# Optimization experiments

Measured on AMD Instinct MI355X. Metric: run time of the kernel, lower is better.

## Reference

```python
import jax, jax.numpy as jnp
import numpy as np

N, E, S = 10000, 100000, 10            # nodes, edges, message-passing steps
NODE_F, EDGE_F, L, H, OUT = 30, 4, 128, 128, 3


def _mlp(h, W0, b0, W1, b1, W2, b2):
    # Linear->ReLU, Linear->ReLU, Linear (build_mlp with num_hidden_layers=2)
    h = jax.nn.relu(h @ W0 + b0)
    h = jax.nn.relu(h @ W1 + b1)
    return h @ W2 + b2


def _ln(h, g, b):
    # torch.nn.LayerNorm over last dim, eps=1e-5, biased variance
    m = h.mean(-1, keepdims=True)
    v = h.var(-1, keepdims=True)
    return (h - m) * jax.lax.rsqrt(v + 1e-5) * g + b


def setup_inputs():
    key = jax.random.key(0)
    ks = iter(jax.random.split(key, 64))

    def w(shape, fan):
        return jax.random.normal(next(ks), shape, dtype=jnp.float32) / np.float32(np.sqrt(fan))

    d = {}
    d["x"] = jax.random.normal(next(ks), (N, NODE_F), dtype=jnp.float32)
    d["ea"] = jax.random.normal(next(ks), (E, EDGE_F), dtype=jnp.float32)
    d["ei"] = jax.random.randint(next(ks), (2, E), 0, N)
    # encoder node ('en') / edge ('ee') MLP+LayerNorm params
    for pre, fin in (("en", NODE_F), ("ee", EDGE_F)):
        d[pre + "W0"] = w((fin, H), fin); d[pre + "b0"] = jnp.zeros((H,), jnp.float32)
        d[pre + "W1"] = w((H, H), H);     d[pre + "b1"] = jnp.zeros((H,), jnp.float32)
        d[pre + "W2"] = w((H, L), H);     d[pre + "b2"] = jnp.zeros((L,), jnp.float32)
        d[pre + "g"] = jnp.ones((L,), jnp.float32); d[pre + "bt"] = jnp.zeros((L,), jnp.float32)
    # processor edge ('pe', in=3L) / node ('pn', in=2L) params, stacked over S steps
    for pre, fin in (("pe", 3 * L), ("pn", 2 * L)):
        d[pre + "W0"] = w((S, fin, H), fin); d[pre + "b0"] = jnp.zeros((S, H), jnp.float32)
        d[pre + "W1"] = w((S, H, H), H);     d[pre + "b1"] = jnp.zeros((S, H), jnp.float32)
        d[pre + "W2"] = w((S, H, L), H);     d[pre + "b2"] = jnp.zeros((S, L), jnp.float32)
        d[pre + "g"] = jnp.ones((S, L), jnp.float32); d[pre + "bt"] = jnp.zeros((S, L), jnp.float32)
    # decoder MLP (no LayerNorm)
    d["dW0"] = w((L, H), L); d["db0"] = jnp.zeros((H,), jnp.float32)
    d["dW1"] = w((H, H), H); d["db1"] = jnp.zeros((H,), jnp.float32)
    d["dW2"] = w((H, OUT), H); d["db2"] = jnp.zeros((OUT,), jnp.float32)
    return d


def reference(x, ea, ei,
              enW0, enb0, enW1, enb1, enW2, enb2, eng, enbt,
              eeW0, eeb0, eeW1, eeb1, eeW2, eeb2, eeg, eebt,
              peW0, peb0, peW1, peb1, peW2, peb2, peg, pebt,
              pnW0, pnb0, pnW1, pnb1, pnW2, pnb2, png, pnbt,
              dW0, db0, dW1, db1, dW2, db2):
    src, dst = ei[0], ei[1]
    # encode (GraphIndependent)
    hx = _ln(_mlp(x, enW0, enb0, enW1, enb1, enW2, enb2), eng, enbt)   # [N, L]
    he = _ln(_mlp(ea, eeW0, eeb0, eeW1, eeb1, eeW2, eeb2), eeg, eebt)  # [E, L]

    # process: S InteractionNetwork steps with residuals
    def step(carry, p):
        cx, ce = carry
        (eW0, eb0, eW1, eb1, eW2, eb2, eg, ebt,
         nW0, nb0, nW1, nb1, nW2, nb2, ng, nbt) = p
        edge_in = jnp.concatenate([cx[src], cx[dst], ce], axis=-1)     # [E, 3L]
        ue = _ln(_mlp(edge_in, eW0, eb0, eW1, eb1, eW2, eb2), eg, ebt)  # [E, L]
        agg = jax.ops.segment_sum(ue, dst, num_segments=N)              # [N, L]
        un = _ln(_mlp(jnp.concatenate([cx, agg], axis=-1), nW0, nb0, nW1, nb1, nW2, nb2), ng, nbt)
        return (cx + un, ce + ue), None

    (hx, he), _ = jax.lax.scan(
        step, (hx, he),
        (peW0, peb0, peW1, peb1, peW2, peb2, peg, pebt,
         pnW0, pnb0, pnW1, pnb1, pnW2, pnb2, png, pnbt))

    # decode
    return _mlp(hx, dW0, db0, dW1, db1, dW2, db2)  # [N, OUT]
```

## Files before the change

kernel.cpp:

```cpp
#include <hip/hip_runtime.h>


#define NN 10000
#define NE 100000
#define STEPS 10
#define NODE_F 30
#define EDGE_F 4
#define L 128
#define AP 132
#define BP 36

#define WS_STRIDE 136
#define AB_STRIDE 136

typedef __bf16 bf16x8 __attribute__((ext_vector_type(8)));
typedef float f32x4 __attribute__((ext_vector_type(4)));

__device__ __forceinline__ unsigned short f2bf(float f) {
  __bf16 b = (__bf16)f;
  return __builtin_bit_cast(unsigned short, b);
}
__device__ __forceinline__ float bf2f(unsigned short u) {
  return __builtin_bit_cast(float, (unsigned)u << 16);
}


__device__ __forceinline__ void stage_W(unsigned short* __restrict__ Ws,
                                        const unsigned short* __restrict__ Wt,
                                        int K, int sec, int tid) {
#pragma unroll
  for (int p = 0; p < 8; ++p) {
    int u = tid + p * 256;
    int n = u >> 4, kk = u & 15;
    uint4 v = *(const uint4*)(Wt + (size_t)n * K + sec * 128 + kk * 8);
    *(uint4*)&Ws[n * WS_STRIDE + kk * 8] = v;
  }
}


__device__ __forceinline__ void init_acc(f32x4 acc[2][4], const float* __restrict__ b,
                                         int wcol, int l16) {
#pragma unroll
  for (int j = 0; j < 4; ++j) {
    float bv = b[wcol + j * 16 + l16];
#pragma unroll
    for (int i = 0; i < 2; ++i) acc[i][j] = f32x4{bv, bv, bv, bv};
  }
}

__device__ __forceinline__ void layer_gbf(const unsigned short* __restrict__ ap0,
                                          const unsigned short* __restrict__ ap1,
                                          const unsigned short* __restrict__ Ws,
                                          f32x4 acc[2][4], int wcol, int l4, int l16) {
#pragma unroll
  for (int kk = 0; kk < 4; ++kk) {
    bf16x8 af[2];
    af[0] = *(const bf16x8*)(ap0 + kk * 32 + l4 * 8);
    af[1] = *(const bf16x8*)(ap1 + kk * 32 + l4 * 8);
#pragma unroll
    for (int j = 0; j < 4; ++j) {
      bf16x8 bv = *(const bf16x8*)&Ws[(wcol + j * 16 + l16) * WS_STRIDE + kk * 32 + l4 * 8];
#pragma unroll
      for (int i = 0; i < 2; ++i)
        acc[i][j] = __builtin_amdgcn_mfma_f32_16x16x32_bf16(af[i], bv, acc[i][j], 0, 0, 0);
    }
  }
}

__device__ __forceinline__ void layer_lds(const unsigned short* __restrict__ Ab,
                                          const unsigned short* __restrict__ Ws,
                                          f32x4 acc[2][4], int wrow, int wcol, int l4, int l16) {
#pragma unroll
  for (int kk = 0; kk < 4; ++kk) {
    bf16x8 af[2];
#pragma unroll
    for (int i = 0; i < 2; ++i)
      af[i] = *(const bf16x8*)&Ab[(wrow + i * 16 + l16) * AB_STRIDE + kk * 32 + l4 * 8];
#pragma unroll
    for (int j = 0; j < 4; ++j) {
      bf16x8 bv = *(const bf16x8*)&Ws[(wcol + j * 16 + l16) * WS_STRIDE + kk * 32 + l4 * 8];
#pragma unroll
      for (int i = 0; i < 2; ++i)
        acc[i][j] = __builtin_amdgcn_mfma_f32_16x16x32_bf16(af[i], bv, acc[i][j], 0, 0, 0);
    }
  }
}

__device__ __forceinline__ void relu_to_Ab(unsigned short* __restrict__ Ab, f32x4 acc[2][4],
                                           int wrow, int wcol, int l4, int l16) {
#pragma unroll
  for (int i = 0; i < 2; ++i)
#pragma unroll
    for (int j = 0; j < 4; ++j)
#pragma unroll
      for (int r = 0; r < 4; ++r) {
        int row = wrow + i * 16 + l4 * 4 + r;
        int col = wcol + j * 16 + l16;
        Ab[row * AB_STRIDE + col] = f2bf(fmaxf(acc[i][j][r], 0.f));
      }
}

__device__ __forceinline__ void ln_partials(const f32x4 acc[2][4], float ps[2][4], float ps2[2][4]) {
#pragma unroll
  for (int i = 0; i < 2; ++i)
#pragma unroll
    for (int r = 0; r < 4; ++r) {
      float s = 0.f, s2 = 0.f;
#pragma unroll
      for (int j = 0; j < 4; ++j) { float v = acc[i][j][r]; s += v; s2 += v * v; }
#pragma unroll
      for (int off = 1; off < 16; off <<= 1) {
        s += __shfl_xor(s, off, 64);
        s2 += __shfl_xor(s2, off, 64);
      }
      ps[i][r] = s; ps2[i][r] = s2;
    }
}


__device__ __forceinline__ void init_acc1(f32x4 acc[4], const float bv[4]) {
#pragma unroll
  for (int j = 0; j < 4; ++j) acc[j] = f32x4{bv[j], bv[j], bv[j], bv[j]};
}

__device__ __forceinline__ void layer_gbf1(const unsigned short* __restrict__ ap,
                                           const unsigned short* __restrict__ Ws,
                                           f32x4 acc[4], int wcol, int l4, int l16) {
#pragma unroll
  for (int kk = 0; kk < 4; ++kk) {
    bf16x8 af = *(const bf16x8*)(ap + kk * 32 + l4 * 8);
#pragma unroll
    for (int j = 0; j < 4; ++j) {
      bf16x8 bv = *(const bf16x8*)&Ws[(wcol + j * 16 + l16) * WS_STRIDE + kk * 32 + l4 * 8];
      acc[j] = __builtin_amdgcn_mfma_f32_16x16x32_bf16(af, bv, acc[j], 0, 0, 0);
    }
  }
}

__device__ __forceinline__ void layer_lds1(const unsigned short* __restrict__ Ab,
                                           const unsigned short* __restrict__ Ws,
                                           f32x4 acc[4], int wrow, int wcol, int l4, int l16) {
#pragma unroll
  for (int kk = 0; kk < 4; ++kk) {
    bf16x8 af = *(const bf16x8*)&Ab[(wrow + l16) * AB_STRIDE + kk * 32 + l4 * 8];
#pragma unroll
    for (int j = 0; j < 4; ++j) {
      bf16x8 bv = *(const bf16x8*)&Ws[(wcol + j * 16 + l16) * WS_STRIDE + kk * 32 + l4 * 8];
      acc[j] = __builtin_amdgcn_mfma_f32_16x16x32_bf16(af, bv, acc[j], 0, 0, 0);
    }
  }
}

__device__ __forceinline__ void relu_to_Ab1(unsigned short* __restrict__ Ab, f32x4 acc[4],
                                            int wrow, int wcol, int l4, int l16) {
#pragma unroll
  for (int j = 0; j < 4; ++j)
#pragma unroll
    for (int r = 0; r < 4; ++r) {
      int row = wrow + l4 * 4 + r;
      int col = wcol + j * 16 + l16;
      Ab[row * AB_STRIDE + col] = f2bf(fmaxf(acc[j][r], 0.f));
    }
}

__device__ __forceinline__ void ln_partials1(const f32x4 acc[4], float ps[4], float ps2[4]) {
#pragma unroll
  for (int r = 0; r < 4; ++r) {
    float s = 0.f, s2 = 0.f;
#pragma unroll
    for (int j = 0; j < 4; ++j) { float v = acc[j][r]; s += v; s2 += v * v; }
#pragma unroll
    for (int off = 1; off < 16; off <<= 1) {
      s += __shfl_xor(s, off, 64);
      s2 += __shfl_xor(s2, off, 64);
    }
    ps[r] = s; ps2[r] = s2;
  }
}


__global__ __launch_bounds__(256) void deg_kernel(const int* __restrict__ ei, int* __restrict__ cnt) {
  int e = blockIdx.x * 256 + threadIdx.x;
  if (e < NE) atomicAdd(&cnt[ei[NE + e]], 1);
}

__global__ __launch_bounds__(256) void scan_kernel(const int* __restrict__ cnt,
                                                   int* __restrict__ off, int* __restrict__ cur) {
  __shared__ int sums[256];
  int t = threadIdx.x;
  int base = t * 40;
  int local = 0;
  for (int i = 0; i < 40; ++i) { int n = base + i; if (n < NN) local += cnt[n]; }
  sums[t] = local;
  __syncthreads();
  int val = local;
  for (int d = 1; d < 256; d <<= 1) {
    int add = (t >= d) ? sums[t - d] : 0;
    __syncthreads();
    sums[t] += add;
    __syncthreads();
  }
  int run = sums[t] - val;
  for (int i = 0; i < 40; ++i) {
    int n = base + i;
    if (n < NN) { off[n] = run; cur[n] = run; run += cnt[n]; }
  }
  if (t == 255) off[NN] = sums[255];
}

__global__ __launch_bounds__(256) void scatter_kernel(const int* __restrict__ ei,
                                                      int* __restrict__ cur, int* __restrict__ eid) {
  int e = blockIdx.x * 256 + threadIdx.x;
  if (e < NE) { int p = atomicAdd(&cur[ei[NE + e]], 1); eid[p] = e; }
}


__global__ __launch_bounds__(256) void edge_step_mfma(
    const unsigned short* __restrict__ hx_bf, unsigned short* __restrict__ he_bf,
    unsigned short* __restrict__ ue_bf,
    const int* __restrict__ ei,
    const unsigned short* __restrict__ W0t, const float* __restrict__ b0,
    const unsigned short* __restrict__ W1t, const float* __restrict__ b1,
    const unsigned short* __restrict__ W2t, const float* __restrict__ b2,
    const float* __restrict__ g, const float* __restrict__ bt) {
  __shared__ __align__(16) unsigned short Ws[128 * WS_STRIDE];
  __shared__ __align__(16) unsigned short Ab[64 * AB_STRIDE];
  __shared__ int sidx[64], didx[64];
  int tid = threadIdx.x;
  int w = tid >> 6, lane = tid & 63;
  int l4 = lane >> 4, l16 = lane & 15;
  int wrow = (w >> 1) * 32, wcol = (w & 1) * 64;
  int e0 = blockIdx.x * 64;
  if (tid < 64) {
    int e = min(e0 + tid, NE - 1);
    sidx[tid] = ei[e];
    didx[tid] = ei[NE + e];
  }
  f32x4 acc[2][4];
  init_acc(acc, b0, wcol, l16);
  __syncthreads();
  for (int sec = 0; sec < 3; ++sec) {
    stage_W(Ws, W0t, 384, sec, tid);
    const unsigned short* ap[2];
#pragma unroll
    for (int i = 0; i < 2; ++i) {
      int r = wrow + i * 16 + l16;
      if (sec == 0)      ap[i] = hx_bf + (size_t)sidx[r] * L;
      else if (sec == 1) ap[i] = hx_bf + (size_t)didx[r] * L;
      else               ap[i] = he_bf + (size_t)min(e0 + r, NE - 1) * L;
    }
    __syncthreads();
    layer_gbf(ap[0], ap[1], Ws, acc, wcol, l4, l16);
    __syncthreads();
  }
  relu_to_Ab(Ab, acc, wrow, wcol, l4, l16);
  stage_W(Ws, W1t, 128, 0, tid);
  init_acc(acc, b1, wcol, l16);
  __syncthreads();
  layer_lds(Ab, Ws, acc, wrow, wcol, l4, l16);
  __syncthreads();
  relu_to_Ab(Ab, acc, wrow, wcol, l4, l16);
  stage_W(Ws, W2t, 128, 0, tid);
  init_acc(acc, b2, wcol, l16);
  __syncthreads();
  layer_lds(Ab, Ws, acc, wrow, wcol, l4, l16);
  float ps[2][4], ps2[2][4];
  ln_partials(acc, ps, ps2);
  __syncthreads();
  float* red = (float*)Ab;
  if (l16 == 0) {
#pragma unroll
    for (int i = 0; i < 2; ++i)
#pragma unroll
      for (int r = 0; r < 4; ++r) {
        int row = wrow + i * 16 + l4 * 4 + r;
        red[(w & 1) * 128 + row * 2 + 0] = ps[i][r];
        red[(w & 1) * 128 + row * 2 + 1] = ps2[i][r];
      }
  }
  __syncthreads();
  float gv[4], btv[4];
#pragma unroll
  for (int j = 0; j < 4; ++j) {
    int col = wcol + j * 16 + l16;
    gv[j] = g[col]; btv[j] = bt[col];
  }
#pragma unroll
  for (int i = 0; i < 2; ++i)
#pragma unroll
    for (int r = 0; r < 4; ++r) {
      int row = wrow + i * 16 + l4 * 4 + r;
      float s  = red[row * 2]     + red[128 + row * 2];
      float s2 = red[row * 2 + 1] + red[128 + row * 2 + 1];
      float m = s * (1.f / 128.f);
      float inv = rsqrtf(s2 * (1.f / 128.f) - m * m + 1e-5f);
      int e = e0 + row;
      if (e < NE) {
        size_t hoff = (size_t)e * L;
#pragma unroll
        for (int j = 0; j < 4; ++j) {
          int col = wcol + j * 16 + l16;
          float u = (acc[i][j][r] - m) * inv * gv[j] + btv[j];
          unsigned short old = he_bf[hoff + col];
          he_bf[hoff + col] = f2bf(bf2f(old) + u);
          ue_bf[hoff + col] = f2bf(u);
        }
      }
    }
}


__global__ __launch_bounds__(256) void node_step_mfma(
    float* __restrict__ hx, unsigned short* __restrict__ hx_bf,
    const unsigned short* __restrict__ ue_bf,
    const int* __restrict__ off, const int* __restrict__ eid,
    const unsigned short* __restrict__ W0t, const float* __restrict__ b0,
    const unsigned short* __restrict__ W1t, const float* __restrict__ b1,
    const unsigned short* __restrict__ W2t, const float* __restrict__ b2,
    const float* __restrict__ g, const float* __restrict__ bt) {
  __shared__ __align__(16) unsigned short Ws[128 * WS_STRIDE];
  __shared__ __align__(16) unsigned short Ab[32 * AB_STRIDE];
  __shared__ __align__(16) unsigned short Ag[32 * AB_STRIDE];
  int tid = threadIdx.x;
  int w = tid >> 6, lane = tid & 63;
  int l4 = lane >> 4, l16 = lane & 15;
  int wrow = (w >> 1) * 16, wcol = (w & 1) * 64;
  int n0 = blockIdx.x * 32;
  {
    int r = tid >> 3;
    int cseg = (tid & 7) * 16;
    int n = n0 + r;
    float a[16];
#pragma unroll
    for (int q = 0; q < 16; ++q) a[q] = 0.f;
    if (n < NN) {
      int p0 = off[n], p1 = off[n + 1];
      for (int p = p0; p < p1; ++p) {
        const unsigned short* row = ue_bf + (size_t)eid[p] * L + cseg;
#pragma unroll
        for (int q = 0; q < 2; ++q) {
          uint4 v = *(const uint4*)(row + q * 8);
          a[q * 8 + 0] += __builtin_bit_cast(float, v.x << 16);
          a[q * 8 + 1] += __builtin_bit_cast(float, v.x & 0xffff0000u);
          a[q * 8 + 2] += __builtin_bit_cast(float, v.y << 16);
          a[q * 8 + 3] += __builtin_bit_cast(float, v.y & 0xffff0000u);
          a[q * 8 + 4] += __builtin_bit_cast(float, v.z << 16);
          a[q * 8 + 5] += __builtin_bit_cast(float, v.z & 0xffff0000u);
          a[q * 8 + 6] += __builtin_bit_cast(float, v.w << 16);
          a[q * 8 + 7] += __builtin_bit_cast(float, v.w & 0xffff0000u);
        }
      }
    }
#pragma unroll
    for (int q = 0; q < 8; ++q) {
      unsigned o = (unsigned)f2bf(a[2 * q]) | ((unsigned)f2bf(a[2 * q + 1]) << 16);
      *(unsigned*)&Ag[r * AB_STRIDE + cseg + 2 * q] = o;
    }
  }
  float bv0[4], bv1[4], bv2[4], gv[4], btv[4];
#pragma unroll
  for (int j = 0; j < 4; ++j) {
    int c = wcol + j * 16 + l16;
    bv0[j] = b0[c]; bv1[j] = b1[c]; bv2[j] = b2[c]; gv[j] = g[c]; btv[j] = bt[c];
  }
  stage_W(Ws, W0t, 256, 0, tid);
  f32x4 acc[4];
  init_acc1(acc, bv0);
  __syncthreads();
  {
    const unsigned short* ap = hx_bf + (size_t)min(n0 + wrow + l16, NN - 1) * L;
    layer_gbf1(ap, Ws, acc, wcol, l4, l16);
  }
  __syncthreads();
  stage_W(Ws, W0t, 256, 1, tid);
  __syncthreads();
  layer_lds1(Ag, Ws, acc, wrow, wcol, l4, l16);
  __syncthreads();
  relu_to_Ab1(Ab, acc, wrow, wcol, l4, l16);
  stage_W(Ws, W1t, 128, 0, tid);
  init_acc1(acc, bv1);
  __syncthreads();
  layer_lds1(Ab, Ws, acc, wrow, wcol, l4, l16);
  __syncthreads();
  relu_to_Ab1(Ab, acc, wrow, wcol, l4, l16);
  stage_W(Ws, W2t, 128, 0, tid);
  init_acc1(acc, bv2);
  __syncthreads();
  layer_lds1(Ab, Ws, acc, wrow, wcol, l4, l16);
  float ps[4], ps2[4];
  ln_partials1(acc, ps, ps2);
  __syncthreads();
  float* red = (float*)Ab;
  if (l16 == 0) {
#pragma unroll
    for (int r = 0; r < 4; ++r) {
      int row = wrow + l4 * 4 + r;
      red[(w & 1) * 64 + row * 2 + 0] = ps[r];
      red[(w & 1) * 64 + row * 2 + 1] = ps2[r];
    }
  }
  __syncthreads();
#pragma unroll
  for (int r = 0; r < 4; ++r) {
    int row = wrow + l4 * 4 + r;
    float s  = red[row * 2]     + red[64 + row * 2];
    float s2 = red[row * 2 + 1] + red[64 + row * 2 + 1];
    float m = s * (1.f / 128.f);
    float inv = rsqrtf(s2 * (1.f / 128.f) - m * m + 1e-5f);
    int n = n0 + row;
    if (n < NN) {
#pragma unroll
      for (int j = 0; j < 4; ++j) {
        int col = wcol + j * 16 + l16;
        float un = (acc[j][r] - m) * inv * gv[j] + btv[j];
        float nv = hx[(size_t)n * L + col] + un;
        hx[(size_t)n * L + col] = nv;
        hx_bf[(size_t)n * L + col] = f2bf(nv);
      }
    }
  }
}


__global__ __launch_bounds__(256) void enc_edge_mfma(
    const float* __restrict__ ea,
    const float* __restrict__ W0, const float* __restrict__ b0,
    const unsigned short* __restrict__ W1t, const float* __restrict__ b1,
    const unsigned short* __restrict__ W2t, const float* __restrict__ b2,
    const float* __restrict__ g, const float* __restrict__ bt,
    unsigned short* __restrict__ he_bf) {
  __shared__ __align__(16) unsigned short Ws[128 * WS_STRIDE];
  __shared__ __align__(16) unsigned short Ab[64 * AB_STRIDE];
  int tid = threadIdx.x;
  int w = tid >> 6, lane = tid & 63;
  int l4 = lane >> 4, l16 = lane & 15;
  int wrow = (w >> 1) * 32, wcol = (w & 1) * 64;
  int e0 = blockIdx.x * 64;
  {
    int row = tid >> 2, cbase = (tid & 3) * 32;
    int e = min(e0 + row, NE - 1);
    float4 eav = *(const float4*)&ea[(size_t)e * 4];
#pragma unroll
    for (int c = 0; c < 32; ++c) {
      int col = cbase + c;
      float sum = b0[col] + eav.x * W0[col] + eav.y * W0[128 + col] +
                  eav.z * W0[256 + col] + eav.w * W0[384 + col];
      Ab[row * AB_STRIDE + col] = f2bf(fmaxf(sum, 0.f));
    }
  }
  stage_W(Ws, W1t, 128, 0, tid);
  f32x4 acc[2][4];
  init_acc(acc, b1, wcol, l16);
  __syncthreads();
  layer_lds(Ab, Ws, acc, wrow, wcol, l4, l16);
  __syncthreads();
  relu_to_Ab(Ab, acc, wrow, wcol, l4, l16);
  stage_W(Ws, W2t, 128, 0, tid);
  init_acc(acc, b2, wcol, l16);
  __syncthreads();
  layer_lds(Ab, Ws, acc, wrow, wcol, l4, l16);
  float ps[2][4], ps2[2][4];
  ln_partials(acc, ps, ps2);
  __syncthreads();
  float* red = (float*)Ws;
  if (l16 == 0) {
#pragma unroll
    for (int i = 0; i < 2; ++i)
#pragma unroll
      for (int r = 0; r < 4; ++r) {
        int row = wrow + i * 16 + l4 * 4 + r;
        red[(w & 1) * 128 + row * 2 + 0] = ps[i][r];
        red[(w & 1) * 128 + row * 2 + 1] = ps2[i][r];
      }
  }
  __syncthreads();
  float gv[4], btv[4];
#pragma unroll
  for (int j = 0; j < 4; ++j) {
    int col = wcol + j * 16 + l16;
    gv[j] = g[col]; btv[j] = bt[col];
  }
#pragma unroll
  for (int i = 0; i < 2; ++i)
#pragma unroll
    for (int r = 0; r < 4; ++r) {
      int row = wrow + i * 16 + l4 * 4 + r;
      float s  = red[row * 2]     + red[128 + row * 2];
      float s2 = red[row * 2 + 1] + red[128 + row * 2 + 1];
      float m = s * (1.f / 128.f);
      float inv = rsqrtf(s2 * (1.f / 128.f) - m * m + 1e-5f);
      int e = e0 + row;
      if (e < NE) {
#pragma unroll
        for (int j = 0; j < 4; ++j) {
          int col = wcol + j * 16 + l16;
          he_bf[(size_t)e * L + col] = f2bf((acc[i][j][r] - m) * inv * gv[j] + btv[j]);
        }
      }
    }
}


__global__ __launch_bounds__(256) void wprep_kernel(
    const float* __restrict__ W0, const float* __restrict__ W1, const float* __restrict__ W2,
    unsigned short* __restrict__ out, int K0, int steps) {
  int per_step = 128 * (K0 + 256);
  int idx = blockIdx.x * 256 + threadIdx.x;
  if (idx >= steps * per_step) return;
  int s = idx / per_step, r = idx - s * per_step;
  float v;
  if (r < 128 * K0) {
    int n = r / K0, k = r - n * K0;
    v = W0[(size_t)s * K0 * 128 + (size_t)k * 128 + n];
  } else {
    r -= 128 * K0;
    const float* W = (r < 16384) ? W1 : W2;
    r &= 16383;
    int n = r >> 7, k = r & 127;
    v = W[(size_t)s * 16384 + k * 128 + n];
  }
  out[idx] = f2bf(v);
}

__global__ __launch_bounds__(256) void tprep_kernel(
    const float* __restrict__ W1, const float* __restrict__ W2, unsigned short* __restrict__ out) {
  int idx = blockIdx.x * 256 + threadIdx.x;
  const float* W = (idx < 16384) ? W1 : W2;
  int r = idx & 16383;
  int n = r >> 7, k = r & 127;
  out[idx] = f2bf(W[k * 128 + n]);
}


__device__ __forceinline__ void load_B(float* __restrict__ Bs, const float* __restrict__ W,
                                       int K, int k0, int tid) {
#pragma unroll
  for (int p = 0; p < 16; ++p) {
    int idx = tid + p * 256;
    int kk = idx >> 7;
    int c = idx & 127;
    float v = 0.f;
    if (k0 + kk < K) v = W[(size_t)(k0 + kk) * L + c];
    Bs[c * BP + kk] = v;
  }
}

__device__ __forceinline__ void fma32(const float* __restrict__ As, const float* __restrict__ Bs,
                                      float acc[4][8], int ty, int tx, int koff) {
#pragma unroll
  for (int kk = 0; kk < 32; kk += 4) {
    float4 a[4];
    float4 b[8];
#pragma unroll
    for (int i = 0; i < 4; ++i)
      a[i] = *(const float4*)&As[(ty + 16 * i) * AP + koff + kk];
#pragma unroll
    for (int j = 0; j < 8; ++j)
      b[j] = *(const float4*)&Bs[(tx + 16 * j) * BP + kk];
#pragma unroll
    for (int i = 0; i < 4; ++i)
#pragma unroll
      for (int j = 0; j < 8; ++j) {
        acc[i][j] = fmaf(a[i].x, b[j].x, acc[i][j]);
        acc[i][j] = fmaf(a[i].y, b[j].y, acc[i][j]);
        acc[i][j] = fmaf(a[i].z, b[j].z, acc[i][j]);
        acc[i][j] = fmaf(a[i].w, b[j].w, acc[i][j]);
      }
  }
}

__device__ __forceinline__ void init_bias(float acc[4][8], const float* __restrict__ b, int tx) {
#pragma unroll
  for (int j = 0; j < 8; ++j) {
    float bv = b[tx + 16 * j];
#pragma unroll
    for (int i = 0; i < 4; ++i) acc[i][j] = bv;
  }
}

__device__ __forceinline__ void store_relu(float* __restrict__ As, float acc[4][8], int ty, int tx) {
#pragma unroll
  for (int i = 0; i < 4; ++i)
#pragma unroll
    for (int j = 0; j < 8; ++j)
      As[(ty + 16 * i) * AP + tx + 16 * j] = fmaxf(acc[i][j], 0.f);
}

__device__ __forceinline__ void layer_As(const float* __restrict__ As, float* __restrict__ Bs,
                                         const float* __restrict__ W, const float* __restrict__ bias,
                                         int K, float acc[4][8], int tid, int ty, int tx) {
  init_bias(acc, bias, tx);
  int nc = (K + 31) >> 5;
  for (int bc = 0; bc < nc; ++bc) {
    __syncthreads();
    load_B(Bs, W, K, bc * 32, tid);
    __syncthreads();
    fma32(As, Bs, acc, ty, tx, bc * 32);
  }
}

__device__ __forceinline__ void fillA_gather(float* __restrict__ As, const float* __restrict__ base,
                                             const int* __restrict__ ridx, int tid) {
#pragma unroll
  for (int p = 0; p < 8; ++p) {
    int idx = tid + p * 256;
    int r = idx >> 5;
    int c4 = idx & 31;
    float4 v = *(const float4*)&base[(size_t)ridx[r] * L + c4 * 4];
    *(float4*)&As[r * AP + c4 * 4] = v;
  }
}

__device__ __forceinline__ void lnorm(float acc[4][8], const float* __restrict__ g,
                                      const float* __restrict__ bt, int tx) {
  float gv[8], bv[8];
#pragma unroll
  for (int j = 0; j < 8; ++j) { gv[j] = g[tx + 16 * j]; bv[j] = bt[tx + 16 * j]; }
#pragma unroll
  for (int i = 0; i < 4; ++i) {
    float s = 0.f, s2 = 0.f;
#pragma unroll
    for (int j = 0; j < 8; ++j) { s += acc[i][j]; s2 += acc[i][j] * acc[i][j]; }
#pragma unroll
    for (int off = 1; off < 16; off <<= 1) {
      s  += __shfl_xor(s, off, 64);
      s2 += __shfl_xor(s2, off, 64);
    }
    float m = s * (1.f / 128.f);
    float var = s2 * (1.f / 128.f) - m * m;
    float inv = rsqrtf(var + 1e-5f);
#pragma unroll
    for (int j = 0; j < 8; ++j) acc[i][j] = (acc[i][j] - m) * inv * gv[j] + bv[j];
  }
}

__global__ __launch_bounds__(256) void enc_node_kernel(
    const float* __restrict__ x,
    const float* __restrict__ W0, const float* __restrict__ b0,
    const float* __restrict__ W1, const float* __restrict__ b1,
    const float* __restrict__ W2, const float* __restrict__ b2,
    const float* __restrict__ g, const float* __restrict__ bt,
    float* __restrict__ hx, unsigned short* __restrict__ hx_bf) {
  __shared__ float As[64 * AP];
  __shared__ float Bs[128 * BP];
  int tid = threadIdx.x, ty = tid >> 4, tx = tid & 15;
  int n0 = blockIdx.x * 64;
#pragma unroll
  for (int p = 0; p < 8; ++p) {
    int idx = tid + p * 256;
    int r = idx >> 5, c = idx & 31;
    int n = min(n0 + r, NN - 1);
    As[r * AP + c] = (c < NODE_F) ? x[(size_t)n * NODE_F + c] : 0.f;
  }
  float acc[4][8];
  init_bias(acc, b0, tx);
  __syncthreads();
  load_B(Bs, W0, NODE_F, 0, tid);
  __syncthreads();
  fma32(As, Bs, acc, ty, tx, 0);

  __syncthreads(); store_relu(As, acc, ty, tx);
  layer_As(As, Bs, W1, b1, L, acc, tid, ty, tx);
  __syncthreads(); store_relu(As, acc, ty, tx);
  layer_As(As, Bs, W2, b2, L, acc, tid, ty, tx);
  lnorm(acc, g, bt, tx);
#pragma unroll
  for (int i = 0; i < 4; ++i) {
    int n = n0 + ty + 16 * i;
    if (n < NN)
#pragma unroll
      for (int j = 0; j < 8; ++j) {
        float v = acc[i][j];
        hx[(size_t)n * L + tx + 16 * j] = v;
        hx_bf[(size_t)n * L + tx + 16 * j] = f2bf(v);
      }
  }
}

__global__ __launch_bounds__(256) void dec_kernel(
    const float* __restrict__ hx,
    const float* __restrict__ W0, const float* __restrict__ b0,
    const float* __restrict__ W1, const float* __restrict__ b1,
    const float* __restrict__ W2, const float* __restrict__ b2,
    float* __restrict__ out) {
  __shared__ float As[64 * AP];
  __shared__ float Bs[128 * BP];
  __shared__ int nidx[64];
  int tid = threadIdx.x, ty = tid >> 4, tx = tid & 15;
  int n0 = blockIdx.x * 64;
  if (tid < 64) nidx[tid] = min(n0 + tid, NN - 1);
  __syncthreads();
  fillA_gather(As, hx, nidx, tid);
  float acc[4][8];
  layer_As(As, Bs, W0, b0, L, acc, tid, ty, tx);
  __syncthreads(); store_relu(As, acc, ty, tx);
  layer_As(As, Bs, W1, b1, L, acc, tid, ty, tx);
  __syncthreads(); store_relu(As, acc, ty, tx);
  __syncthreads();
  if (tid < 192) {
    int r = tid / 3, o = tid - (tid / 3) * 3;
    int n = n0 + r;
    if (n < NN) {
      float s = b2[o];
#pragma unroll 8
      for (int k = 0; k < L; ++k) s = fmaf(As[r * AP + k], W2[k * 3 + o], s);
      out[(size_t)n * 3 + o] = s;
    }
  }
}


extern "C" void kernel_launch(void* const* d_in, const int* in_sizes, int n_in,
                              void* d_out, int out_size, void* d_ws, size_t ws_size,
                              hipStream_t stream) {
  (void)in_sizes; (void)n_in; (void)out_size; (void)ws_size;
  const float* x    = (const float*)d_in[0];
  const float* ea   = (const float*)d_in[1];
  const int*   ei   = (const int*)d_in[2];
  const float* enW0 = (const float*)d_in[3];  const float* enb0 = (const float*)d_in[4];
  const float* enW1 = (const float*)d_in[5];  const float* enb1 = (const float*)d_in[6];
  const float* enW2 = (const float*)d_in[7];  const float* enb2 = (const float*)d_in[8];
  const float* eng  = (const float*)d_in[9];  const float* enbt = (const float*)d_in[10];
  const float* eeW0 = (const float*)d_in[11]; const float* eeb0 = (const float*)d_in[12];
  const float* eeW1 = (const float*)d_in[13]; const float* eeb1 = (const float*)d_in[14];
  const float* eeW2 = (const float*)d_in[15]; const float* eeb2 = (const float*)d_in[16];
  const float* eeg  = (const float*)d_in[17]; const float* eebt = (const float*)d_in[18];
  const float* peW0 = (const float*)d_in[19]; const float* peb0 = (const float*)d_in[20];
  const float* peW1 = (const float*)d_in[21]; const float* peb1 = (const float*)d_in[22];
  const float* peW2 = (const float*)d_in[23]; const float* peb2 = (const float*)d_in[24];
  const float* peg  = (const float*)d_in[25]; const float* pebt = (const float*)d_in[26];
  const float* pnW0 = (const float*)d_in[27]; const float* pnb0 = (const float*)d_in[28];
  const float* pnW1 = (const float*)d_in[29]; const float* pnb1 = (const float*)d_in[30];
  const float* pnW2 = (const float*)d_in[31]; const float* pnb2 = (const float*)d_in[32];
  const float* png  = (const float*)d_in[33]; const float* pnbt = (const float*)d_in[34];
  const float* dW0  = (const float*)d_in[35]; const float* db0  = (const float*)d_in[36];
  const float* dW1  = (const float*)d_in[37]; const float* db1  = (const float*)d_in[38];
  const float* dW2  = (const float*)d_in[39]; const float* db2  = (const float*)d_in[40];

  const size_t F_HX = (size_t)NN * L, F_HE = (size_t)NE * L;
  const size_t W_PE = 819200, W_PN = 655360, W_EE = 32768;

  float* hx = (float*)d_ws;
  unsigned short* he_bf  = (unsigned short*)(hx + F_HX);
  unsigned short* ue_bf  = he_bf + F_HE;
  unsigned short* hx_bf  = ue_bf + F_HE;
  unsigned short* wt_pe  = hx_bf + F_HX;
  unsigned short* wt_pn  = wt_pe + W_PE;
  unsigned short* wt_ee  = wt_pn + W_PN;
  int* cnt = (int*)(wt_ee + W_EE);
  int* off = cnt + NN;
  int* cur = off + NN + 1;
  int* eid = cur + NN;

  dim3 blk(256);
  int grid_n64 = (NN + 63) / 64;
  int grid_n32 = (NN + 31) / 32;
  int grid_e   = (NE + 63) / 64;

  wprep_kernel<<<(10 * 81920 + 255) / 256, blk, 0, stream>>>(peW0, peW1, peW2, wt_pe, 384, 10);
  wprep_kernel<<<(10 * 65536 + 255) / 256, blk, 0, stream>>>(pnW0, pnW1, pnW2, wt_pn, 256, 10);
  tprep_kernel<<<128, blk, 0, stream>>>(eeW1, eeW2, wt_ee);

  hipMemsetAsync(cnt, 0, (size_t)NN * 4, stream);
  deg_kernel<<<(NE + 255) / 256, blk, 0, stream>>>(ei, cnt);
  scan_kernel<<<1, blk, 0, stream>>>(cnt, off, cur);
  scatter_kernel<<<(NE + 255) / 256, blk, 0, stream>>>(ei, cur, eid);

  enc_node_kernel<<<grid_n64, blk, 0, stream>>>(x, enW0, enb0, enW1, enb1, enW2, enb2, eng, enbt, hx, hx_bf);
  enc_edge_mfma<<<grid_e, blk, 0, stream>>>(ea, eeW0, eeb0, wt_ee, eeb1, wt_ee + 16384, eeb2, eeg, eebt, he_bf);

  for (int s = 0; s < STEPS; ++s) {
    const unsigned short* pe = wt_pe + (size_t)s * 81920;
    const unsigned short* pn = wt_pn + (size_t)s * 65536;
    edge_step_mfma<<<grid_e, blk, 0, stream>>>(
        hx_bf, he_bf, ue_bf, ei,
        pe,                 peb0 + (size_t)s * L,
        pe + 49152,         peb1 + (size_t)s * L,
        pe + 49152 + 16384, peb2 + (size_t)s * L,
        peg + (size_t)s * L, pebt + (size_t)s * L);
    node_step_mfma<<<grid_n32, blk, 0, stream>>>(
        hx, hx_bf, ue_bf, off, eid,
        pn,                 pnb0 + (size_t)s * L,
        pn + 32768,         pnb1 + (size_t)s * L,
        pn + 32768 + 16384, pnb2 + (size_t)s * L,
        png + (size_t)s * L, pnbt + (size_t)s * L);
  }

  dec_kernel<<<grid_n64, blk, 0, stream>>>(hx, dW0, db0, dW1, db1, dW2, db2, (float*)d_out);
}
```

Measured before the change: 921.5 us.

## Double edge-step tile to 128 edges per block with 4x4 MFMA subtiles

The edge-step kernel now processes 128 edges per block instead of 64. Each wave computes a 64x64 output tile with 4x4 MFMA accumulators, so every staged weight tile in LDS is reused across twice as many rows. Bias, gamma and beta loads are hoisted to the kernel start, and the LayerNorm reduction buffer moves into the weight LDS area. The cost is more accumulator registers per thread, a larger LDS footprint and half as many blocks, which may lower occupancy and latency hiding for the gathered loads.

```diff
diff --git a/kernel.cpp b/kernel.cpp
--- a/kernel.cpp
+++ b/kernel.cpp
@@ -103,6 +103,85 @@
 __device__ __forceinline__ void ln_partials(const f32x4 acc[2][4], float ps[2][4], float ps2[2][4]) {
 #pragma unroll
   for (int i = 0; i < 2; ++i)
+#pragma unroll
+    for (int r = 0; r < 4; ++r) {
+      float s = 0.f, s2 = 0.f;
+#pragma unroll
+      for (int j = 0; j < 4; ++j) { float v = acc[i][j][r]; s += v; s2 += v * v; }
+#pragma unroll
+      for (int off = 1; off < 16; off <<= 1) {
+        s += __shfl_xor(s, off, 64);
+        s2 += __shfl_xor(s2, off, 64);
+      }
+      ps[i][r] = s; ps2[i][r] = s2;
+    }
+}
+
+
+__device__ __forceinline__ void init_acc4(f32x4 acc[4][4], const float bv[4]) {
+#pragma unroll
+  for (int j = 0; j < 4; ++j) {
+    f32x4 b = {bv[j], bv[j], bv[j], bv[j]};
+#pragma unroll
+    for (int i = 0; i < 4; ++i) acc[i][j] = b;
+  }
+}
+
+__device__ __forceinline__ void layer_gbf4(const unsigned short* const ap[4],
+                                           const unsigned short* __restrict__ Ws,
+                                           f32x4 acc[4][4], int wcol, int l4, int l16) {
+#pragma unroll
+  for (int kk = 0; kk < 4; ++kk) {
+    bf16x8 af[4];
+#pragma unroll
+    for (int i = 0; i < 4; ++i)
+      af[i] = *(const bf16x8*)(ap[i] + kk * 32 + l4 * 8);
+#pragma unroll
+    for (int j = 0; j < 4; ++j) {
+      bf16x8 bv = *(const bf16x8*)&Ws[(wcol + j * 16 + l16) * WS_STRIDE + kk * 32 + l4 * 8];
+#pragma unroll
+      for (int i = 0; i < 4; ++i)
+        acc[i][j] = __builtin_amdgcn_mfma_f32_16x16x32_bf16(af[i], bv, acc[i][j], 0, 0, 0);
+    }
+  }
+}
+
+__device__ __forceinline__ void layer_lds4(const unsigned short* __restrict__ Ab,
+                                           const unsigned short* __restrict__ Ws,
+                                           f32x4 acc[4][4], int wrow, int wcol, int l4, int l16) {
+#pragma unroll
+  for (int kk = 0; kk < 4; ++kk) {
+    bf16x8 af[4];
+#pragma unroll
+    for (int i = 0; i < 4; ++i)
+      af[i] = *(const bf16x8*)&Ab[(wrow + i * 16 + l16) * AB_STRIDE + kk * 32 + l4 * 8];
+#pragma unroll
+    for (int j = 0; j < 4; ++j) {
+      bf16x8 bv = *(const bf16x8*)&Ws[(wcol + j * 16 + l16) * WS_STRIDE + kk * 32 + l4 * 8];
+#pragma unroll
+      for (int i = 0; i < 4; ++i)
+        acc[i][j] = __builtin_amdgcn_mfma_f32_16x16x32_bf16(af[i], bv, acc[i][j], 0, 0, 0);
+    }
+  }
+}
+
+__device__ __forceinline__ void relu_to_Ab4(unsigned short* __restrict__ Ab, f32x4 acc[4][4],
+                                            int wrow, int wcol, int l4, int l16) {
+#pragma unroll
+  for (int i = 0; i < 4; ++i)
+#pragma unroll
+    for (int j = 0; j < 4; ++j)
+#pragma unroll
+      for (int r = 0; r < 4; ++r) {
+        int row = wrow + i * 16 + l4 * 4 + r;
+        int col = wcol + j * 16 + l16;
+        Ab[row * AB_STRIDE + col] = f2bf(fmaxf(acc[i][j][r], 0.f));
+      }
+}
+
+__device__ __forceinline__ void ln_partials4(const f32x4 acc[4][4], float ps[4][4], float ps2[4][4]) {
+#pragma unroll
+  for (int i = 0; i < 4; ++i)
 #pragma unroll
     for (int r = 0; r < 4; ++r) {
       float s = 0.f, s2 = 0.f;
@@ -224,74 +303,74 @@
     const unsigned short* __restrict__ W2t, const float* __restrict__ b2,
     const float* __restrict__ g, const float* __restrict__ bt) {
   __shared__ __align__(16) unsigned short Ws[128 * WS_STRIDE];
-  __shared__ __align__(16) unsigned short Ab[64 * AB_STRIDE];
-  __shared__ int sidx[64], didx[64];
+  __shared__ __align__(16) unsigned short Ab[128 * AB_STRIDE];
+  __shared__ int sidx[128], didx[128];
   int tid = threadIdx.x;
   int w = tid >> 6, lane = tid & 63;
   int l4 = lane >> 4, l16 = lane & 15;
-  int wrow = (w >> 1) * 32, wcol = (w & 1) * 64;
-  int e0 = blockIdx.x * 64;
-  if (tid < 64) {
+  int wrow = (w >> 1) * 64, wcol = (w & 1) * 64;
+  int e0 = blockIdx.x * 128;
+  if (tid < 128) {
     int e = min(e0 + tid, NE - 1);
     sidx[tid] = ei[e];
     didx[tid] = ei[NE + e];
   }
-  f32x4 acc[2][4];
-  init_acc(acc, b0, wcol, l16);
+  float bv0[4], bv1[4], bv2[4], gv[4], btv[4];
+#pragma unroll
+  for (int j = 0; j < 4; ++j) {
+    int c = wcol + j * 16 + l16;
+    bv0[j] = b0[c]; bv1[j] = b1[c]; bv2[j] = b2[c]; gv[j] = g[c]; btv[j] = bt[c];
+  }
+  f32x4 acc[4][4];
+  init_acc4(acc, bv0);
   __syncthreads();
   for (int sec = 0; sec < 3; ++sec) {
     stage_W(Ws, W0t, 384, sec, tid);
-    const unsigned short* ap[2];
-#pragma unroll
-    for (int i = 0; i < 2; ++i) {
+    const unsigned short* ap[4];
+#pragma unroll
+    for (int i = 0; i < 4; ++i) {
       int r = wrow + i * 16 + l16;
       if (sec == 0)      ap[i] = hx_bf + (size_t)sidx[r] * L;
       else if (sec == 1) ap[i] = hx_bf + (size_t)didx[r] * L;
       else               ap[i] = he_bf + (size_t)min(e0 + r, NE - 1) * L;
     }
     __syncthreads();
-    layer_gbf(ap[0], ap[1], Ws, acc, wcol, l4, l16);
+    layer_gbf4(ap, Ws, acc, wcol, l4, l16);
     __syncthreads();
   }
-  relu_to_Ab(Ab, acc, wrow, wcol, l4, l16);
+  relu_to_Ab4(Ab, acc, wrow, wcol, l4, l16);
   stage_W(Ws, W1t, 128, 0, tid);
-  init_acc(acc, b1, wcol, l16);
-  __syncthreads();
-  layer_lds(Ab, Ws, acc, wrow, wcol, l4, l16);
-  __syncthreads();
-  relu_to_Ab(Ab, acc, wrow, wcol, l4, l16);
+  init_acc4(acc, bv1);
+  __syncthreads();
+  layer_lds4(Ab, Ws, acc, wrow, wcol, l4, l16);
+  __syncthreads();
+  relu_to_Ab4(Ab, acc, wrow, wcol, l4, l16);
   stage_W(Ws, W2t, 128, 0, tid);
-  init_acc(acc, b2, wcol, l16);
-  __syncthreads();
-  layer_lds(Ab, Ws, acc, wrow, wcol, l4, l16);
-  float ps[2][4], ps2[2][4];
-  ln_partials(acc, ps, ps2);
-  __syncthreads();
-  float* red = (float*)Ab;
+  init_acc4(acc, bv2);
+  __syncthreads();
+  layer_lds4(Ab, Ws, acc, wrow, wcol, l4, l16);
+  float ps[4][4], ps2[4][4];
+  ln_partials4(acc, ps, ps2);
+  __syncthreads();
+  float* red = (float*)Ws;
   if (l16 == 0) {
 #pragma unroll
-    for (int i = 0; i < 2; ++i)
+    for (int i = 0; i < 4; ++i)
 #pragma unroll
       for (int r = 0; r < 4; ++r) {
         int row = wrow + i * 16 + l4 * 4 + r;
-        red[(w & 1) * 128 + row * 2 + 0] = ps[i][r];
-        red[(w & 1) * 128 + row * 2 + 1] = ps2[i][r];
-      }
-  }
-  __syncthreads();
-  float gv[4], btv[4];
-#pragma unroll
-  for (int j = 0; j < 4; ++j) {
-    int col = wcol + j * 16 + l16;
-    gv[j] = g[col]; btv[j] = bt[col];
-  }
-#pragma unroll
-  for (int i = 0; i < 2; ++i)
+        red[(w & 1) * 256 + row * 2 + 0] = ps[i][r];
+        red[(w & 1) * 256 + row * 2 + 1] = ps2[i][r];
+      }
+  }
+  __syncthreads();
+#pragma unroll
+  for (int i = 0; i < 4; ++i)
 #pragma unroll
     for (int r = 0; r < 4; ++r) {
       int row = wrow + i * 16 + l4 * 4 + r;
-      float s  = red[row * 2]     + red[128 + row * 2];
-      float s2 = red[row * 2 + 1] + red[128 + row * 2 + 1];
+      float s  = red[row * 2]     + red[256 + row * 2];
+      float s2 = red[row * 2 + 1] + red[256 + row * 2 + 1];
       float m = s * (1.f / 128.f);
       float inv = rsqrtf(s2 * (1.f / 128.f) - m * m + 1e-5f);
       int e = e0 + row;
@@ -753,9 +832,10 @@
   int* eid = cur + NN;
 
   dim3 blk(256);
-  int grid_n64 = (NN + 63) / 64;
-  int grid_n32 = (NN + 31) / 32;
-  int grid_e   = (NE + 63) / 64;
+  int grid_n64  = (NN + 63) / 64;
+  int grid_n32  = (NN + 31) / 32;
+  int grid_e64  = (NE + 63) / 64;
+  int grid_e128 = (NE + 127) / 128;
 
   wprep_kernel<<<(10 * 81920 + 255) / 256, blk, 0, stream>>>(peW0, peW1, peW2, wt_pe, 384, 10);
   wprep_kernel<<<(10 * 65536 + 255) / 256, blk, 0, stream>>>(pnW0, pnW1, pnW2, wt_pn, 256, 10);
@@ -767,12 +847,12 @@
   scatter_kernel<<<(NE + 255) / 256, blk, 0, stream>>>(ei, cur, eid);
 
   enc_node_kernel<<<grid_n64, blk, 0, stream>>>(x, enW0, enb0, enW1, enb1, enW2, enb2, eng, enbt, hx, hx_bf);
-  enc_edge_mfma<<<grid_e, blk, 0, stream>>>(ea, eeW0, eeb0, wt_ee, eeb1, wt_ee + 16384, eeb2, eeg, eebt, he_bf);
+  enc_edge_mfma<<<grid_e64, blk, 0, stream>>>(ea, eeW0, eeb0, wt_ee, eeb1, wt_ee + 16384, eeb2, eeg, eebt, he_bf);
 
   for (int s = 0; s < STEPS; ++s) {
     const unsigned short* pe = wt_pe + (size_t)s * 81920;
     const unsigned short* pn = wt_pn + (size_t)s * 65536;
-    edge_step_mfma<<<grid_e, blk, 0, stream>>>(
+    edge_step_mfma<<<grid_e128, blk, 0, stream>>>(
         hx_bf, he_bf, ue_bf, ei,
         pe,                 peb0 + (size_t)s * L,
         pe + 49152,         peb1 + (size_t)s * L,
```

Measured after the change: 1.491 ms. 1.62x slower.
